# Performance work log

Hardware: AMD Instinct MI355X
Metric: run time of the kernel (lower is better)

## Reference

```python
import jax, jax.numpy as jnp
import numpy as np

GAMMA = 2.0
ALPHA_CLASS = 0.01
ALPHA_COORD = 1.0

def _xywh_to_xyxy(b):
    # [.., 4] (x, y, w, h) -> (x1, y1, x2, y2)
    return jnp.concatenate([b[..., :2], b[..., :2] + b[..., 2:]], axis=-1)

def _jaccard(a, b):
    # a: [A,4] xyxy, b: [N,4] xyxy -> IoU [A,N]
    lt = jnp.maximum(a[:, None, :2], b[None, :, :2])
    rb = jnp.minimum(a[:, None, 2:], b[None, :, 2:])
    wh = jnp.clip(rb - lt, 0.0)
    inter = wh[..., 0] * wh[..., 1]
    area_a = (a[:, 2] - a[:, 0]) * (a[:, 3] - a[:, 1])
    area_b = (b[:, 2] - b[:, 0]) * (b[:, 3] - b[:, 1])
    return inter / (area_a[:, None] + area_b[None, :] - inter)

def _match_mask(thr, anchors, gt_xywh, num_obj):
    # Returns positive (anchor, gt) pair mask [A, N_max], honoring gt[:num_obj].
    A = anchors.shape[0]
    N = gt_xywh.shape[0]
    gt_boxes = _xywh_to_xyxy(gt_xywh)
    ious = _jaccard(anchors, gt_boxes)              # [A, N]
    valid = jnp.arange(N) < num_obj                 # [N]
    ious_v = jnp.where(valid[None, :], ious, -jnp.inf)
    best_gt_idx = jnp.argmax(ious_v, axis=0)        # [N] best anchor per gt
    forced = jnp.arange(A)[:, None] == best_gt_idx[None, :]  # positive_mask[best,i]=1
    return ((ious > thr) | forced) & valid[None, :]

def _class_loss_item(thr, classes, anchors, gt, num_obj):
    # classes: [A,2] probs (col0 = background, col1 = face)
    mask = _match_mask(thr, anchors, gt, num_obj)   # [A, N]
    counts = jnp.sum(mask, axis=1)                  # [A] multiplicity of each anchor in positive_idx
    is_pos = counts > 0                             # dedup, as index_fill_ does
    probs = jnp.where(is_pos, classes[:, 1], classes[:, 0])
    focal = -((1.0 - probs) ** GAMMA) * jnp.log(probs)
    # extra = focal_loss.index_select(0, positive_idx) keeps duplicates -> weight by counts
    extra = jnp.sum(counts.astype(focal.dtype) * focal)
    return jnp.sum(focal) + 10.0 * extra

def setup_inputs() -> dict:
    key = jax.random.key(0)
    B, A, N = 16, 131072, 64
    k1, k2, k3, k4, k5, k6 = jax.random.split(key, 6)
    # anchors in xyxy, valid boxes in [0,1]
    a_xy = jax.random.uniform(k1, (A, 2), jnp.float32, 0.0, 0.8)
    a_wh = jax.random.uniform(k2, (A, 2), jnp.float32, 0.05, 0.2)
    anchors = jnp.concatenate([a_xy, a_xy + a_wh], axis=-1)
    # class probabilities strictly in (0,1) for log()
    batch_classes = jax.random.uniform(k3, (B, A, 2), jnp.float32, 0.05, 0.95)
    g_xy = jax.random.uniform(k4, (B, N, 2), jnp.float32, 0.0, 0.8)
    g_wh = jax.random.uniform(k5, (B, N, 2), jnp.float32, 0.05, 0.2)
    batch_gt = jnp.concatenate([g_xy, g_wh], axis=-1)  # xywh
    batch_num_objects = jax.random.randint(k6, (B,), 1, N + 1, jnp.int32)
    return {
        "threshhold": jnp.float32(0.5),
        "batch_classes": batch_classes,
        "anchors": anchors,
        "batch_gt": batch_gt,
        "batch_num_objects": batch_num_objects,
    }

def reference(threshhold, batch_classes, anchors, batch_gt, batch_num_objects):
    R = batch_classes.shape[0]
    per_item = jax.vmap(lambda c, g, n: _class_loss_item(threshhold, c, anchors, g, n))
    class_loss = jnp.sum(per_item(batch_classes, batch_gt, batch_num_objects))
    class_loss = class_loss * ALPHA_CLASS / R
    # Faithful to the source: coord_loss is initialized to zero and never accumulated
    coord_loss = jnp.zeros((), batch_classes.dtype) * ALPHA_COORD / R
    total_loss = class_loss + coord_loss
    return (total_loss, class_loss, coord_loss)
```

## Files before the change

### kernel.cpp

```cpp
#include <hip/hip_runtime.h>

typedef unsigned long long ull;

#define NANCH    131072
#define NMAX     64
#define NBATCH   16
#define THREADS  256
#define APT      4
#define ACH      (THREADS*APT)
#define NPAIR    8
#define NB_CNT   ((NANCH/ACH)*NPAIR)
#define AC_ANCH  256
#define BPB_A    128
#define MAXB     16
#define NB_ARG   (MAXB*BPB_A)
#define GRID_MAIN (NB_CNT+NB_ARG)


__device__ __forceinline__ float focal_f(float p) {
    float om = 1.0f - p;
    return -om * om * __logf(p);
}

__global__ __launch_bounds__(64) void k_setup(
    const int* __restrict__ nobj, ull* __restrict__ cells,
    int* __restrict__ pairs, int* __restrict__ lanepk, int* __restrict__ nbund)
{
    int tid = threadIdx.x;
    for (int i = tid; i < NBATCH*NMAX; i += 64) cells[i] = 0ull;
    for (int i = tid; i < MAXB*NMAX; i += 64) lanepk[i] = -1;

    __shared__ int s_b[NBATCH], s_no[NBATCH], s_bu[NBATCH], s_st[NBATCH];
    if (tid == 0) {
        int ord[NBATCH], key[NBATCH];
        for (int i = 0; i < NBATCH; ++i) { ord[i] = i; key[i] = nobj[i]; }
        for (int i = 1; i < NBATCH; ++i) {
            int k = key[i], o = ord[i], j = i-1;
            while (j >= 0 && key[j] < k) { key[j+1]=key[j]; ord[j+1]=ord[j]; --j; }
            key[j+1] = k; ord[j+1] = o;
        }
        for (int p = 0; p < NPAIR; ++p) {
            pairs[2*p]   = ord[p];
            pairs[2*p+1] = ord[NBATCH-1-p];
        }
        int rem[MAXB]; int nb = 0;
        for (int i = 0; i < NBATCH; ++i) {
            int n = key[i], f = -1;
            for (int x = 0; x < nb; ++x) if (rem[x] >= n) { f = x; break; }
            if (f < 0) { f = nb++; rem[f] = NMAX; }
            s_b[i] = ord[i]; s_no[i] = n; s_bu[i] = f; s_st[i] = NMAX - rem[f];
            rem[f] -= n;
        }
        *nbund = nb;
    }
    __syncthreads();
    #pragma unroll
    for (int i = 0; i < NBATCH; ++i) {
        if (tid < s_no[i])
            lanepk[s_bu[i]*NMAX + s_st[i] + tid] = (s_b[i] << 8) | tid;
    }
}

__global__ __launch_bounds__(THREADS) void k_main(
    const float* __restrict__ thr_p,
    const float* __restrict__ classes,
    const float* __restrict__ anchors,
    const float* __restrict__ gt,
    const int*   __restrict__ nobj,
    const int*   __restrict__ pairs,
    const int*   __restrict__ lanepk,
    const int*   __restrict__ nbund,
    ull* __restrict__ cells,
    double* __restrict__ partials)
{
    int bid0 = blockIdx.x;
    int tid  = threadIdx.x;
    float thr = *thr_p;
    float q   = thr / (1.0f + thr);
    bool is_cnt = (bid0 % 3) == 0;
    int  bid    = is_cnt ? (bid0 / 3) : ((bid0 / 3) * 2 + (bid0 % 3) - 1);

    if (is_cnt) {
        int chunk = bid >> 3, pr = bid & 7;
        int b0 = pairs[2*pr], b1 = pairs[2*pr+1];
        int no0 = nobj[b0], no1 = nobj[b1];

        __shared__ float4 sbox[2*NMAX];
        __shared__ float  sqg[2*NMAX];
        __shared__ double sw[4];
        if (tid < 2*NMAX) {
            int s = tid >> 6, n = tid & 63;
            int b  = s ? b1 : b0;
            int no = s ? no1 : no0;
            float4 g = reinterpret_cast<const float4*>(gt)[b*NMAX + n];
            float x2 = g.x + g.z, y2 = g.y + g.w;
            float4 box = make_float4(g.x, g.y, x2, y2);
            float  qg  = q * ((x2 - g.x) * (y2 - g.y));
            if (n >= no) { box = make_float4(4.f,4.f,4.f,4.f); qg = __builtin_inff(); }
            sbox[tid] = box; sqg[tid] = qg;
        }
        __syncthreads();

        float ax1[APT], ay1[APT], ax2[APT], ay2[APT], qa[APT];
        int abase = chunk * ACH + tid;
        #pragma unroll
        for (int k = 0; k < APT; ++k) {
            float4 v = reinterpret_cast<const float4*>(anchors)[abase + k*THREADS];
            ax1[k]=v.x; ay1[k]=v.y; ax2[k]=v.z; ay2[k]=v.w;
            qa[k] = q * ((v.z - v.x) * (v.w - v.y));
        }

        int wv = tid >> 6, ln = tid & 63;
        double acc = 0.0;
        #pragma unroll
        for (int s = 0; s < 2; ++s) {
            int b    = s ? b1 : b0;
            int no   = s ? no1 : no0;
            int no4  = (no + 3) & ~3;
            int base = s * NMAX;
            int cnt[APT];
            #pragma unroll
            for (int k = 0; k < APT; ++k) cnt[k] = 0;

            for (int n = 0; n < no4; n += 4) {
                #pragma unroll
                for (int u = 0; u < 4; ++u) {
                    float4 g  = sbox[base + n + u];
                    float  qg = sqg[base + n + u];
                    #pragma unroll
                    for (int k = 0; k < APT; ++k) {
                        float lx = fmaxf(ax1[k], g.x);
                        float ly = fmaxf(ay1[k], g.y);
                        float rx = fminf(ax2[k], g.z);
                        float ry = fminf(ay2[k], g.w);
                        float w  = fmaxf(rx - lx, 0.f);
                        float h  = fmaxf(ry - ly, 0.f);
                        float inter = w * h;
                        cnt[k] += (inter > qa[k] + qg) ? 1 : 0;
                    }
                }
            }
            const float2* cp = reinterpret_cast<const float2*>(classes) + (size_t)b * NANCH;
            #pragma unroll
            for (int k = 0; k < APT; ++k) {
                float2 c = cp[abase + k*THREADS];
                float p  = (cnt[k] > 0) ? c.y : c.x;
                float f  = focal_f(p);
                acc += (double)(f * (1.0f + 10.0f * (float)cnt[k]));
            }
        }
        #pragma unroll
        for (int off = 32; off; off >>= 1) acc += __shfl_xor(acc, off, 64);
        if (ln == 0) sw[wv] = acc;
        __syncthreads();
        if (tid == 0) partials[bid] = sw[0] + sw[1] + sw[2] + sw[3];

    } else {
        int bu   = bid >> 7;
        int blkc = bid & (BPB_A - 1);
        if (bu >= *nbund) return;
        int wv = tid >> 6, ln = tid & 63;
        int abase = (blkc*4 + wv) * AC_ANCH;

        int lp = lanepk[bu*NMAX + ln];
        bool valid = lp >= 0;
        int gidx = valid ? ((lp >> 8)*NMAX + (lp & 255)) : 0;
        float4 gg = reinterpret_cast<const float4*>(gt)[gidx];
        float gx2 = gg.x + gg.z, gy2 = gg.y + gg.w;
        float gar = (gx2 - gg.x) * (gy2 - gg.y);

        float bn[8], bs[8]; int bj[8];
        #pragma unroll
        for (int u = 0; u < 8; ++u) { bn[u] = -1.f; bs[u] = 1.f; bj[u] = 0; }
        const float4* ap = reinterpret_cast<const float4*>(anchors) + abase;

        float4 va[4], vb[4];
        #pragma unroll
        for (int u = 0; u < 4; ++u) va[u] = ap[u];
        #pragma unroll
        for (int u = 0; u < 4; ++u) vb[u] = ap[4 + u];
        for (int j = 0; j < AC_ANCH; j += 8) {
            int jn = (j + 8 < AC_ANCH) ? (j + 8) : j;
            #pragma unroll
            for (int u = 0; u < 4; ++u) {
                float4 v = va[u];
                float aar = (v.z - v.x) * (v.w - v.y);
                float lx = fmaxf(v.x, gg.x), ly = fmaxf(v.y, gg.y);
                float rx = fminf(v.z, gx2),  ry = fminf(v.w, gy2);
                float w  = fmaxf(rx - lx, 0.f), h = fmaxf(ry - ly, 0.f);
                float inter = w * h;
                float sa    = aar + gar;
                bool better = inter * bs[u] > bn[u] * sa;
                bn[u] = better ? inter : bn[u];
                bs[u] = better ? sa    : bs[u];
                bj[u] = better ? (j+u) : bj[u];
            }
            #pragma unroll
            for (int u = 0; u < 4; ++u) va[u] = ap[jn + u];
            #pragma unroll
            for (int u = 0; u < 4; ++u) {
                float4 v = vb[u];
                float aar = (v.z - v.x) * (v.w - v.y);
                float lx = fmaxf(v.x, gg.x), ly = fmaxf(v.y, gg.y);
                float rx = fminf(v.z, gx2),  ry = fminf(v.w, gy2);
                float w  = fmaxf(rx - lx, 0.f), h = fmaxf(ry - ly, 0.f);
                float inter = w * h;
                float sa    = aar + gar;
                int c = 4 + u;
                bool better = inter * bs[c] > bn[c] * sa;
                bn[c] = better ? inter     : bn[c];
                bs[c] = better ? sa        : bs[c];
                bj[c] = better ? (j+4+u)   : bj[c];
            }
            #pragma unroll
            for (int u = 0; u < 4; ++u) vb[u] = ap[jn + 4 + u];
        }
        if (valid) {
            ull best = 0;
            #pragma unroll
            for (int u = 0; u < 8; ++u) {
                float rr = bn[u] * __builtin_amdgcn_rcpf(bs[u]);
                unsigned aidx = (unsigned)(abase + bj[u]);
                ull pk = ((ull)__float_as_uint(rr) << 32)
                       | (ull)(0x7FFFFFFFu - aidx);
                best = pk > best ? pk : best;
            }
            atomicMax(&cells[(lp >> 8)*NMAX + (lp & 255)], best);
        }
    }
}

__global__ __launch_bounds__(1024) void k_tail(
    const float* __restrict__ thr_p,
    const float* __restrict__ classes,
    const float* __restrict__ anchors,
    const float* __restrict__ gt,
    const int*   __restrict__ nobj,
    const ull*   __restrict__ cells,
    const double* __restrict__ partials,
    float* __restrict__ out)
{
    int tid = threadIdx.x;
    int b = tid >> 6, n = tid & 63;
    float thr = *thr_p;
    float q   = thr / (1.0f + thr);

    __shared__ float4 sbox[NBATCH*NMAX];
    __shared__ float  sqg[NBATCH*NMAX];
    __shared__ int    sidx[NBATCH*NMAX];
    __shared__ double sdelta[NBATCH];
    __shared__ double sw[16];

    int n_obj = nobj[b];
    {
        float4 g = reinterpret_cast<const float4*>(gt)[b*NMAX + n];
        float x2 = g.x + g.z, y2 = g.y + g.w;
        sbox[tid] = make_float4(g.x, g.y, x2, y2);
        float gar = (x2 - g.x) * (y2 - g.y);
        sqg[tid]  = q * gar;
    }
    __syncthreads();

    int bi = -1; bool need = false;
    float4 av = make_float4(0.f,0.f,0.f,0.f);
    float qa = 0.f;
    if (n < n_obj) {
        ull pkv = cells[tid];
        bi = (int)(0x7FFFFFFFu - (unsigned)(pkv & 0xFFFFFFFFull));
        av = reinterpret_cast<const float4*>(anchors)[bi];
        float aar = (av.z - av.x) * (av.w - av.y);
        qa = q * aar;
        float4 g = sbox[tid];
        float lx = fmaxf(av.x, g.x), ly = fmaxf(av.y, g.y);
        float rx = fminf(av.z, g.z), ry = fminf(av.w, g.w);
        float w  = fmaxf(rx - lx, 0.f), h = fmaxf(ry - ly, 0.f);
        float inter = w * h;
        need = !(inter > qa + sqg[tid]);
    }
    sidx[tid] = need ? bi : -1;
    __syncthreads();

    double delta = 0.0;
    if (need) {
        bool first = true; int extra = 0;
        int base = b * NMAX;
        for (int m = 0; m < NMAX; ++m) {
            if (sidx[base + m] == bi) { if (m < n) first = false; ++extra; }
        }
        if (first) {
            int count = 0;
            for (int m = 0; m < n_obj; ++m) {
                float4 g = sbox[base + m];
                float lx = fmaxf(av.x, g.x), ly = fmaxf(av.y, g.y);
                float rx = fminf(av.z, g.z), ry = fminf(av.w, g.w);
                float w  = fmaxf(rx - lx, 0.f), h = fmaxf(ry - ly, 0.f);
                float inter = w * h;
                count += (inter > qa + sqg[base + m]) ? 1 : 0;
            }
            float2 c = reinterpret_cast<const float2*>(classes)[(size_t)b * NANCH + bi];
            float po = (count > 0) ? c.y : c.x;
            float fo = focal_f(po);
            float oldc = fo * (1.0f + 10.0f * (float)count);
            int cn = count + extra;
            float pn = (cn > 0) ? c.y : c.x;
            float fn = focal_f(pn);
            float newc = fn * (1.0f + 10.0f * (float)cn);
            delta = (double)newc - (double)oldc;
        }
    }
    #pragma unroll
    for (int off = 32; off; off >>= 1) delta += __shfl_xor(delta, off, 64);
    if (n == 0) sdelta[b] = delta;
    __syncthreads();

    double v = partials[tid];
    if (tid < NBATCH) v += sdelta[tid];
    #pragma unroll
    for (int off = 32; off; off >>= 1) v += __shfl_xor(v, off, 64);
    if ((tid & 63) == 0) sw[tid >> 6] = v;
    __syncthreads();
    if (tid == 0) {
        double tot = 0.0;
        #pragma unroll
        for (int i = 0; i < 16; ++i) tot += sw[i];
        double cls = tot * (0.01 / 16.0);
        out[0] = (float)cls;
        out[1] = (float)cls;
        out[2] = 0.0f;
    }
}

extern "C" void kernel_launch(void* const* d_in, const int* in_sizes, int n_in,
                              void* d_out, int out_size, void* d_ws, size_t ws_size,
                              hipStream_t stream) {
    const float* thr     = (const float*)d_in[0];
    const float* classes = (const float*)d_in[1];
    const float* anchors = (const float*)d_in[2];
    const float* gt      = (const float*)d_in[3];
    const int*   nobj    = (const int*)d_in[4];
    float* out = (float*)d_out;

    char* ws = (char*)d_ws;
    ull*    cells    = (ull*)(ws + 0);
    int*    pairs    = (int*)(ws + 8192);
    int*    lanepk   = (int*)(ws + 8256);
    int*    nbund    = (int*)(ws + 12352);
    double* partials = (double*)(ws + 12416);

    k_setup<<<1, 64, 0, stream>>>(nobj, cells, pairs, lanepk, nbund);
    k_main<<<GRID_MAIN, THREADS, 0, stream>>>(thr, classes, anchors, gt, nobj,
                                              pairs, lanepk, nbund, cells, partials);
    k_tail<<<1, 1024, 0, stream>>>(thr, classes, anchors, gt, nobj, cells, partials, out);
}
```

Before: 95.53 us.

## Fuse tail into main kernel via last-block ticket; one batch per count block

The tail kernel is removed. Its fix-up work now runs in whichever main-kernel block finishes last, detected through an atomic counter after a threadfence. The count blocks now each handle a single batch instead of a sorted pair, and count and argmax blocks are interleaved even/odd. Cells and the counter are zeroed with a memset instead of inside the setup kernel. The aim is to save a kernel launch and its gap, at the cost of a serial tail inside the last block and an extra memset node.

```diff
diff --git a/kernel.cpp b/kernel.cpp
--- a/kernel.cpp
+++ b/kernel.cpp
@@ -8,8 +8,8 @@
 #define THREADS  256
 #define APT      4
 #define ACH      (THREADS*APT)
-#define NPAIR    8
-#define NB_CNT   ((NANCH/ACH)*NPAIR)
+#define NCHUNK   (NANCH/ACH)
+#define NB_CNT   (NCHUNK*NBATCH)
 #define AC_ANCH  256
 #define BPB_A    128
 #define MAXB     16
@@ -23,13 +23,10 @@
 }
 
 __global__ __launch_bounds__(64) void k_setup(
-    const int* __restrict__ nobj, ull* __restrict__ cells,
-    int* __restrict__ pairs, int* __restrict__ lanepk, int* __restrict__ nbund)
+    const int* __restrict__ nobj, int* __restrict__ lanepk, int* __restrict__ nbund)
 {
     int tid = threadIdx.x;
-    for (int i = tid; i < NBATCH*NMAX; i += 64) cells[i] = 0ull;
     for (int i = tid; i < MAXB*NMAX; i += 64) lanepk[i] = -1;
-
     __shared__ int s_b[NBATCH], s_no[NBATCH], s_bu[NBATCH], s_st[NBATCH];
     if (tid == 0) {
         int ord[NBATCH], key[NBATCH];
@@ -39,10 +36,6 @@
             while (j >= 0 && key[j] < k) { key[j+1]=key[j]; ord[j+1]=ord[j]; --j; }
             key[j+1] = k; ord[j+1] = o;
         }
-        for (int p = 0; p < NPAIR; ++p) {
-            pairs[2*p]   = ord[p];
-            pairs[2*p+1] = ord[NBATCH-1-p];
-        }
         int rem[MAXB]; int nb = 0;
         for (int i = 0; i < NBATCH; ++i) {
             int n = key[i], f = -1;
@@ -55,10 +48,9 @@
     }
     __syncthreads();
     #pragma unroll
-    for (int i = 0; i < NBATCH; ++i) {
+    for (int i = 0; i < NBATCH; ++i)
         if (tid < s_no[i])
             lanepk[s_bu[i]*NMAX + s_st[i] + tid] = (s_b[i] << 8) | tid;
-    }
 }
 
 __global__ __launch_bounds__(THREADS) void k_main(
@@ -67,36 +59,35 @@
     const float* __restrict__ anchors,
     const float* __restrict__ gt,
     const int*   __restrict__ nobj,
-    const int*   __restrict__ pairs,
     const int*   __restrict__ lanepk,
     const int*   __restrict__ nbund,
     ull* __restrict__ cells,
-    double* __restrict__ partials)
+    double* __restrict__ partials,
+    int* __restrict__ done,
+    float* __restrict__ out)
 {
-    int bid0 = blockIdx.x;
-    int tid  = threadIdx.x;
+    __shared__ float4 sbox[2*NMAX];
+    __shared__ float  sqg[2*NMAX];
+    __shared__ int    sidx2[2*NMAX];
+    __shared__ int    snob[2];
+    __shared__ double sw[4];
+    __shared__ int    s_last;
+
+    int bid = blockIdx.x, tid = threadIdx.x;
+    int wv = tid >> 6, ln = tid & 63;
     float thr = *thr_p;
     float q   = thr / (1.0f + thr);
-    bool is_cnt = (bid0 % 3) == 0;
-    int  bid    = is_cnt ? (bid0 / 3) : ((bid0 / 3) * 2 + (bid0 % 3) - 1);
-
-    if (is_cnt) {
-        int chunk = bid >> 3, pr = bid & 7;
-        int b0 = pairs[2*pr], b1 = pairs[2*pr+1];
-        int no0 = nobj[b0], no1 = nobj[b1];
-
-        __shared__ float4 sbox[2*NMAX];
-        __shared__ float  sqg[2*NMAX];
-        __shared__ double sw[4];
-        if (tid < 2*NMAX) {
-            int s = tid >> 6, n = tid & 63;
-            int b  = s ? b1 : b0;
-            int no = s ? no1 : no0;
-            float4 g = reinterpret_cast<const float4*>(gt)[b*NMAX + n];
+
+    if ((bid & 1) == 0) {
+        int cbid  = bid >> 1;
+        int chunk = cbid >> 4, b = cbid & 15;
+        int no = nobj[b];
+        if (tid < NMAX) {
+            float4 g = reinterpret_cast<const float4*>(gt)[b*NMAX + tid];
             float x2 = g.x + g.z, y2 = g.y + g.w;
             float4 box = make_float4(g.x, g.y, x2, y2);
             float  qg  = q * ((x2 - g.x) * (y2 - g.y));
-            if (n >= no) { box = make_float4(4.f,4.f,4.f,4.f); qg = __builtin_inff(); }
+            if (tid >= no) { box = make_float4(4.f,4.f,4.f,4.f); qg = __builtin_inff(); }
             sbox[tid] = box; sqg[tid] = qg;
         }
         __syncthreads();
@@ -110,220 +101,196 @@
             qa[k] = q * ((v.z - v.x) * (v.w - v.y));
         }
 
-        int wv = tid >> 6, ln = tid & 63;
+        int no4 = (no + 3) & ~3;
+        int cnt[APT];
+        #pragma unroll
+        for (int k = 0; k < APT; ++k) cnt[k] = 0;
+        for (int n = 0; n < no4; n += 4) {
+            #pragma unroll
+            for (int u = 0; u < 4; ++u) {
+                float4 g  = sbox[n + u];
+                float  qg = sqg[n + u];
+                #pragma unroll
+                for (int k = 0; k < APT; ++k) {
+                    float lx = fmaxf(ax1[k], g.x);
+                    float ly = fmaxf(ay1[k], g.y);
+                    float rx = fminf(ax2[k], g.z);
+                    float ry = fminf(ay2[k], g.w);
+                    float w  = fmaxf(rx - lx, 0.f);
+                    float h  = fmaxf(ry - ly, 0.f);
+                    float inter = w * h;
+                    cnt[k] += (inter > qa[k] + qg) ? 1 : 0;
+                }
+            }
+        }
         double acc = 0.0;
+        const float2* cp = reinterpret_cast<const float2*>(classes) + (size_t)b * NANCH;
         #pragma unroll
-        for (int s = 0; s < 2; ++s) {
-            int b    = s ? b1 : b0;
-            int no   = s ? no1 : no0;
-            int no4  = (no + 3) & ~3;
-            int base = s * NMAX;
-            int cnt[APT];
-            #pragma unroll
-            for (int k = 0; k < APT; ++k) cnt[k] = 0;
-
-            for (int n = 0; n < no4; n += 4) {
-                #pragma unroll
-                for (int u = 0; u < 4; ++u) {
-                    float4 g  = sbox[base + n + u];
-                    float  qg = sqg[base + n + u];
-                    #pragma unroll
-                    for (int k = 0; k < APT; ++k) {
-                        float lx = fmaxf(ax1[k], g.x);
-                        float ly = fmaxf(ay1[k], g.y);
-                        float rx = fminf(ax2[k], g.z);
-                        float ry = fminf(ay2[k], g.w);
-                        float w  = fmaxf(rx - lx, 0.f);
-                        float h  = fmaxf(ry - ly, 0.f);
-                        float inter = w * h;
-                        cnt[k] += (inter > qa[k] + qg) ? 1 : 0;
-                    }
-                }
-            }
-            const float2* cp = reinterpret_cast<const float2*>(classes) + (size_t)b * NANCH;
-            #pragma unroll
-            for (int k = 0; k < APT; ++k) {
-                float2 c = cp[abase + k*THREADS];
-                float p  = (cnt[k] > 0) ? c.y : c.x;
-                float f  = focal_f(p);
-                acc += (double)(f * (1.0f + 10.0f * (float)cnt[k]));
-            }
+        for (int k = 0; k < APT; ++k) {
+            float2 c = cp[abase + k*THREADS];
+            float p  = (cnt[k] > 0) ? c.y : c.x;
+            acc += (double)(focal_f(p) * (1.0f + 10.0f * (float)cnt[k]));
         }
         #pragma unroll
         for (int off = 32; off; off >>= 1) acc += __shfl_xor(acc, off, 64);
         if (ln == 0) sw[wv] = acc;
         __syncthreads();
-        if (tid == 0) partials[bid] = sw[0] + sw[1] + sw[2] + sw[3];
+        if (tid == 0) partials[cbid] = sw[0] + sw[1] + sw[2] + sw[3];
 
     } else {
-        int bu   = bid >> 7;
-        int blkc = bid & (BPB_A - 1);
-        if (bu >= *nbund) return;
-        int wv = tid >> 6, ln = tid & 63;
-        int abase = (blkc*4 + wv) * AC_ANCH;
-
-        int lp = lanepk[bu*NMAX + ln];
-        bool valid = lp >= 0;
-        int gidx = valid ? ((lp >> 8)*NMAX + (lp & 255)) : 0;
-        float4 gg = reinterpret_cast<const float4*>(gt)[gidx];
-        float gx2 = gg.x + gg.z, gy2 = gg.y + gg.w;
-        float gar = (gx2 - gg.x) * (gy2 - gg.y);
-
-        float bn[8], bs[8]; int bj[8];
-        #pragma unroll
-        for (int u = 0; u < 8; ++u) { bn[u] = -1.f; bs[u] = 1.f; bj[u] = 0; }
-        const float4* ap = reinterpret_cast<const float4*>(anchors) + abase;
-
-        float4 va[4], vb[4];
-        #pragma unroll
-        for (int u = 0; u < 4; ++u) va[u] = ap[u];
-        #pragma unroll
-        for (int u = 0; u < 4; ++u) vb[u] = ap[4 + u];
-        for (int j = 0; j < AC_ANCH; j += 8) {
-            int jn = (j + 8 < AC_ANCH) ? (j + 8) : j;
+        int abid = bid >> 1;
+        int bu   = abid >> 7;
+        int blkc = abid & (BPB_A - 1);
+        if (bu < *nbund) {
+            int abase = (blkc*4 + wv) * AC_ANCH;
+            int lp = lanepk[bu*NMAX + ln];
+            bool valid = lp >= 0;
+            int gidx = valid ? ((lp >> 8)*NMAX + (lp & 255)) : 0;
+            float4 gg = reinterpret_cast<const float4*>(gt)[gidx];
+            float gx2 = gg.x + gg.z, gy2 = gg.y + gg.w;
+            float gar = (gx2 - gg.x) * (gy2 - gg.y);
+
+            float bn[8], bs[8]; int bj[8];
             #pragma unroll
-            for (int u = 0; u < 4; ++u) {
-                float4 v = va[u];
-                float aar = (v.z - v.x) * (v.w - v.y);
-                float lx = fmaxf(v.x, gg.x), ly = fmaxf(v.y, gg.y);
-                float rx = fminf(v.z, gx2),  ry = fminf(v.w, gy2);
-                float w  = fmaxf(rx - lx, 0.f), h = fmaxf(ry - ly, 0.f);
-                float inter = w * h;
-                float sa    = aar + gar;
-                bool better = inter * bs[u] > bn[u] * sa;
-                bn[u] = better ? inter : bn[u];
-                bs[u] = better ? sa    : bs[u];
-                bj[u] = better ? (j+u) : bj[u];
-            }
+            for (int u = 0; u < 8; ++u) { bn[u] = -1.f; bs[u] = 1.f; bj[u] = 0; }
+            const float4* ap = reinterpret_cast<const float4*>(anchors) + abase;
+
+            float4 va[4], vb[4];
             #pragma unroll
-            for (int u = 0; u < 4; ++u) va[u] = ap[jn + u];
+            for (int u = 0; u < 4; ++u) va[u] = ap[u];
             #pragma unroll
-            for (int u = 0; u < 4; ++u) {
-                float4 v = vb[u];
-                float aar = (v.z - v.x) * (v.w - v.y);
-                float lx = fmaxf(v.x, gg.x), ly = fmaxf(v.y, gg.y);
-                float rx = fminf(v.z, gx2),  ry = fminf(v.w, gy2);
-                float w  = fmaxf(rx - lx, 0.f), h = fmaxf(ry - ly, 0.f);
-                float inter = w * h;
-                float sa    = aar + gar;
-                int c = 4 + u;
-                bool better = inter * bs[c] > bn[c] * sa;
-                bn[c] = better ? inter     : bn[c];
-                bs[c] = better ? sa        : bs[c];
-                bj[c] = better ? (j+4+u)   : bj[c];
-            }
-            #pragma unroll
-            for (int u = 0; u < 4; ++u) vb[u] = ap[jn + 4 + u];
-        }
-        if (valid) {
-            ull best = 0;
-            #pragma unroll
-            for (int u = 0; u < 8; ++u) {
-                float rr = bn[u] * __builtin_amdgcn_rcpf(bs[u]);
-                unsigned aidx = (unsigned)(abase + bj[u]);
-                ull pk = ((ull)__float_as_uint(rr) << 32)
-                       | (ull)(0x7FFFFFFFu - aidx);
-                best = pk > best ? pk : best;
-            }
-            atomicMax(&cells[(lp >> 8)*NMAX + (lp & 255)], best);
-        }
-    }
-}
-
-__global__ __launch_bounds__(1024) void k_tail(
-    const float* __restrict__ thr_p,
-    const float* __restrict__ classes,
-    const float* __restrict__ anchors,
-    const float* __restrict__ gt,
-    const int*   __restrict__ nobj,
-    const ull*   __restrict__ cells,
-    const double* __restrict__ partials,
-    float* __restrict__ out)
-{
-    int tid = threadIdx.x;
-    int b = tid >> 6, n = tid & 63;
-    float thr = *thr_p;
-    float q   = thr / (1.0f + thr);
-
-    __shared__ float4 sbox[NBATCH*NMAX];
-    __shared__ float  sqg[NBATCH*NMAX];
-    __shared__ int    sidx[NBATCH*NMAX];
-    __shared__ double sdelta[NBATCH];
-    __shared__ double sw[16];
-
-    int n_obj = nobj[b];
-    {
-        float4 g = reinterpret_cast<const float4*>(gt)[b*NMAX + n];
-        float x2 = g.x + g.z, y2 = g.y + g.w;
-        sbox[tid] = make_float4(g.x, g.y, x2, y2);
-        float gar = (x2 - g.x) * (y2 - g.y);
-        sqg[tid]  = q * gar;
+            for (int u = 0; u < 4; ++u) vb[u] = ap[4 + u];
+            for (int j = 0; j < AC_ANCH; j += 8) {
+                int jn = (j + 8 < AC_ANCH) ? (j + 8) : j;
+                #pragma unroll
+                for (int u = 0; u < 4; ++u) {
+                    float4 v = va[u];
+                    float aar = (v.z - v.x) * (v.w - v.y);
+                    float lx = fmaxf(v.x, gg.x), ly = fmaxf(v.y, gg.y);
+                    float rx = fminf(v.z, gx2),  ry = fminf(v.w, gy2);
+                    float w  = fmaxf(rx - lx, 0.f), h = fmaxf(ry - ly, 0.f);
+                    float inter = w * h;
+                    float sa    = aar + gar;
+                    bool better = inter * bs[u] > bn[u] * sa;
+                    bn[u] = better ? inter : bn[u];
+                    bs[u] = better ? sa    : bs[u];
+                    bj[u] = better ? (j+u) : bj[u];
+                }
+                #pragma unroll
+                for (int u = 0; u < 4; ++u) va[u] = ap[jn + u];
+                #pragma unroll
+                for (int u = 0; u < 4; ++u) {
+                    float4 v = vb[u];
+                    float aar = (v.z - v.x) * (v.w - v.y);
+                    float lx = fmaxf(v.x, gg.x), ly = fmaxf(v.y, gg.y);
+                    float rx = fminf(v.z, gx2),  ry = fminf(v.w, gy2);
+                    float w  = fmaxf(rx - lx, 0.f), h = fmaxf(ry - ly, 0.f);
+                    float inter = w * h;
+                    float sa    = aar + gar;
+                    int c = 4 + u;
+                    bool better = inter * bs[c] > bn[c] * sa;
+                    bn[c] = better ? inter   : bn[c];
+                    bs[c] = better ? sa      : bs[c];
+                    bj[c] = better ? (j+4+u) : bj[c];
+                }
+                #pragma unroll
+                for (int u = 0; u < 4; ++u) vb[u] = ap[jn + 4 + u];
+            }
+            if (valid) {
+                ull best = 0;
+                #pragma unroll
+                for (int u = 0; u < 8; ++u) {
+                    float rr = bn[u] * __builtin_amdgcn_rcpf(bs[u]);
+                    unsigned aidx = (unsigned)(abase + bj[u]);
+                    ull pk = ((ull)__float_as_uint(rr) << 32)
+                           | (ull)(0x7FFFFFFFu - aidx);
+                    best = pk > best ? pk : best;
+                }
+                atomicMax(&cells[(lp >> 8)*NMAX + (lp & 255)], best);
+            }
+        }
+    }
+
+    __threadfence();
+    if (tid == 0) {
+        int old = atomicAdd(done, 1);
+        s_last = (old == GRID_MAIN - 1) ? 1 : 0;
     }
     __syncthreads();
-
-    int bi = -1; bool need = false;
-    float4 av = make_float4(0.f,0.f,0.f,0.f);
-    float qa = 0.f;
-    if (n < n_obj) {
-        ull pkv = cells[tid];
-        bi = (int)(0x7FFFFFFFu - (unsigned)(pkv & 0xFFFFFFFFull));
-        av = reinterpret_cast<const float4*>(anchors)[bi];
-        float aar = (av.z - av.x) * (av.w - av.y);
-        qa = q * aar;
-        float4 g = sbox[tid];
-        float lx = fmaxf(av.x, g.x), ly = fmaxf(av.y, g.y);
-        float rx = fminf(av.z, g.z), ry = fminf(av.w, g.w);
-        float w  = fmaxf(rx - lx, 0.f), h = fmaxf(ry - ly, 0.f);
-        float inter = w * h;
-        need = !(inter > qa + sqg[tid]);
-    }
-    sidx[tid] = need ? bi : -1;
-    __syncthreads();
-
-    double delta = 0.0;
-    if (need) {
-        bool first = true; int extra = 0;
-        int base = b * NMAX;
-        for (int m = 0; m < NMAX; ++m) {
-            if (sidx[base + m] == bi) { if (m < n) first = false; ++extra; }
-        }
-        if (first) {
-            int count = 0;
-            for (int m = 0; m < n_obj; ++m) {
-                float4 g = sbox[base + m];
-                float lx = fmaxf(av.x, g.x), ly = fmaxf(av.y, g.y);
-                float rx = fminf(av.z, g.z), ry = fminf(av.w, g.w);
-                float w  = fmaxf(rx - lx, 0.f), h = fmaxf(ry - ly, 0.f);
-                float inter = w * h;
-                count += (inter > qa + sqg[base + m]) ? 1 : 0;
-            }
-            float2 c = reinterpret_cast<const float2*>(classes)[(size_t)b * NANCH + bi];
-            float po = (count > 0) ? c.y : c.x;
-            float fo = focal_f(po);
-            float oldc = fo * (1.0f + 10.0f * (float)count);
-            int cn = count + extra;
-            float pn = (cn > 0) ? c.y : c.x;
-            float fn = focal_f(pn);
-            float newc = fn * (1.0f + 10.0f * (float)cn);
-            delta = (double)newc - (double)oldc;
-        }
-    }
+    if (!s_last) return;
+    __threadfence();
+
+    double dacc = 0.0;
+    for (int pb = 0; pb < 8; ++pb) {
+        if (tid < 2*NMAX) {
+            int h = tid >> 6, n = tid & 63;
+            int b = 2*pb + h;
+            float4 g = reinterpret_cast<const float4*>(gt)[b*NMAX + n];
+            float x2 = g.x + g.z, y2 = g.y + g.w;
+            sbox[tid] = make_float4(g.x, g.y, x2, y2);
+            sqg[tid]  = q * ((x2 - g.x) * (y2 - g.y));
+            if (n == 0) snob[h] = nobj[b];
+        }
+        __syncthreads();
+
+        int bi = -1; bool need = false;
+        float4 av = make_float4(0.f,0.f,0.f,0.f);
+        float qa = 0.f;
+        int h = tid >> 6, n = tid & 63, b = 2*pb + h;
+        if (tid < 2*NMAX && n < snob[h]) {
+            ull pkv = cells[b*NMAX + n];
+            bi = (int)(0x7FFFFFFFu - (unsigned)(pkv & 0xFFFFFFFFull));
+            av = reinterpret_cast<const float4*>(anchors)[bi];
+            float aar = (av.z - av.x) * (av.w - av.y);
+            qa = q * aar;
+            float4 g = sbox[tid];
+            float lx = fmaxf(av.x, g.x), ly = fmaxf(av.y, g.y);
+            float rx = fminf(av.z, g.z), ry = fminf(av.w, g.w);
+            float w  = fmaxf(rx - lx, 0.f), hh = fmaxf(ry - ly, 0.f);
+            float inter = w * hh;
+            need = !(inter > qa + sqg[tid]);
+        }
+        if (tid < 2*NMAX) sidx2[tid] = need ? bi : -1;
+        __syncthreads();
+
+        if (need) {
+            bool first = true; int extra = 0;
+            int base = h * NMAX;
+            for (int m = 0; m < NMAX; ++m) {
+                if (sidx2[base + m] == bi) { if (m < n) first = false; ++extra; }
+            }
+            if (first) {
+                int no = snob[h];
+                int count = 0;
+                for (int m = 0; m < no; ++m) {
+                    float4 g = sbox[base + m];
+                    float lx = fmaxf(av.x, g.x), ly = fmaxf(av.y, g.y);
+                    float rx = fminf(av.z, g.z), ry = fminf(av.w, g.w);
+                    float w  = fmaxf(rx - lx, 0.f), hh = fmaxf(ry - ly, 0.f);
+                    float inter = w * hh;
+                    count += (inter > qa + sqg[base + m]) ? 1 : 0;
+                }
+                float2 c = reinterpret_cast<const float2*>(classes)[(size_t)b * NANCH + bi];
+                float po = (count > 0) ? c.y : c.x;
+                float oldc = focal_f(po) * (1.0f + 10.0f * (float)count);
+                int cn = count + extra;
+                float pn = (cn > 0) ? c.y : c.x;
+                float newc = focal_f(pn) * (1.0f + 10.0f * (float)cn);
+                dacc += (double)newc - (double)oldc;
+            }
+        }
+        __syncthreads();
+    }
+
+    double v = dacc;
     #pragma unroll
-    for (int off = 32; off; off >>= 1) delta += __shfl_xor(delta, off, 64);
-    if (n == 0) sdelta[b] = delta;
-    __syncthreads();
-
-    double v = partials[tid];
-    if (tid < NBATCH) v += sdelta[tid];
+    for (int k = 0; k < 8; ++k) v += partials[tid + k*256];
     #pragma unroll
     for (int off = 32; off; off >>= 1) v += __shfl_xor(v, off, 64);
-    if ((tid & 63) == 0) sw[tid >> 6] = v;
+    if (ln == 0) sw[wv] = v;
     __syncthreads();
     if (tid == 0) {
-        double tot = 0.0;
-        #pragma unroll
-        for (int i = 0; i < 16; ++i) tot += sw[i];
-        double cls = tot * (0.01 / 16.0);
+        double cls = (sw[0] + sw[1] + sw[2] + sw[3]) * (0.01 / 16.0);
         out[0] = (float)cls;
         out[1] = (float)cls;
         out[2] = 0.0f;
@@ -342,13 +309,14 @@
 
     char* ws = (char*)d_ws;
     ull*    cells    = (ull*)(ws + 0);
-    int*    pairs    = (int*)(ws + 8192);
+    int*    done     = (int*)(ws + 8192);
     int*    lanepk   = (int*)(ws + 8256);
     int*    nbund    = (int*)(ws + 12352);
     double* partials = (double*)(ws + 12416);
 
-    k_setup<<<1, 64, 0, stream>>>(nobj, cells, pairs, lanepk, nbund);
+    hipMemsetAsync(ws, 0, 8256, stream);
+    k_setup<<<1, 64, 0, stream>>>(nobj, lanepk, nbund);
     k_main<<<GRID_MAIN, THREADS, 0, stream>>>(thr, classes, anchors, gt, nobj,
-                                              pairs, lanepk, nbund, cells, partials);
-    k_tail<<<1, 1024, 0, stream>>>(thr, classes, anchors, gt, nobj, cells, partials, out);
+                                              lanepk, nbund, cells, partials,
+                                              done, out);
 }
```

New measurement: 359.0 us. +275.8%, slower.
